# Optimization experiments

Measured on AMD Instinct MI355X. Metric: run time of the kernel, lower is better.

Reference implementation:

```python
import jax, jax.numpy as jnp
import numpy as np

B, S, D = 32, 512, 1024
H, HD = 16, 64          # num_heads, head_dim
K = 64                  # downsampling_k
NEG = -9e15             # -9000000000000000.0 in source


def setup_inputs() -> dict:
    key0 = jax.random.key(0)
    ks = jax.random.split(key0, 8)
    glorot = lambda k, shape, fan: jax.random.uniform(k, shape, jnp.float32,
                                                      -np.sqrt(6.0 / fan), np.sqrt(6.0 / fan))
    fan = D + H * HD  # glorot_uniform over (hidden, heads*head_dim)
    return {
        "query": jax.random.normal(ks[0], (B, S, D), jnp.float32),
        "key": jax.random.normal(ks[1], (B, S, D), jnp.float32),
        "value": jax.random.normal(ks[2], (B, S, D), jnp.float32),
        "query_kernel": glorot(ks[3], (D, H, HD), fan),
        "key_kernel": glorot(ks[4], (D, H, HD), fan),
        "value_kernel": glorot(ks[5], (D, H, HD), fan),
        "key_downsample_mat": (1.0 / K) * jax.random.normal(ks[6], (K, S), jnp.float32),
        "value_downsample_mat": (1.0 / K) * jax.random.normal(ks[7], (K, S), jnp.float32),
    }


def reference(query, key, value, query_kernel, key_kernel, value_kernel,
              key_downsample_mat, value_downsample_mat):
    # Linformer-style downsampling of K/V along the sequence axis: [B,S,D] -> [B,K,D]
    key_ds = jnp.einsum('ks,bsd->bkd', key_downsample_mat, key)
    val_ds = jnp.einsum('ks,bsd->bkd', value_downsample_mat, value)

    # Per-head projections
    q = jnp.einsum('bsd,dnh->bsnh', query, query_kernel)   # [B,S,H,HD]
    k = jnp.einsum('bkd,dnh->bknh', key_ds, key_kernel)    # [B,K,H,HD]
    v = jnp.einsum('bkd,dnh->bknh', val_ds, value_kernel)  # [B,K,H,HD]

    # Masked softmax attention over the downsampled key set
    scores = jnp.einsum('bqnh,bknh->bnqk', q, k)           # [B,H,S,K]
    # Source builds tril over [S, K_down] then slices first K cols (no-op here)
    mask = jnp.tril(jnp.ones((S, K), dtype=bool))          # [S,K], broadcasts over B,H
    scores = jnp.where(mask, scores, NEG)
    attn = jax.nn.softmax(scores, axis=-1)                 # dropout deterministic (train=False)

    a_v = jnp.einsum('bnqk,bknh->bqnh', attn, v)           # [B,S,H,HD]
    return a_v.reshape(B, S, H * HD)
```

## Files before the change

kernel.cpp:

```cpp
#include <hip/hip_runtime.h>
#include <stdint.h>

#define B_   32
#define S_   512
#define D_   1024
#define H_   16
#define HD_  64
#define KD_  64
#define NH_  1024

typedef __attribute__((ext_vector_type(8))) short short8;
typedef __attribute__((ext_vector_type(4))) float floatx4;

#define GAS __attribute__((address_space(1)))
#define LAS __attribute__((address_space(3)))

__device__ __forceinline__ ushort f2bf(float f) {
  uint32_t u = __float_as_uint(f);
  u = u + 0x7FFFu + ((u >> 16) & 1u);
  return (ushort)(u >> 16);
}

__device__ __forceinline__ float bf2f(ushort h) {
  return __uint_as_float(((uint32_t)h) << 16);
}

__device__ __forceinline__ void gload_lds16(const void* g, void* l) {
  __builtin_amdgcn_global_load_lds((const GAS uint32_t*)g, (LAS uint32_t*)l, 16, 0, 0);
}

#define BARRIER() asm volatile("s_barrier" ::: "memory")
#define WAITLGKM() asm volatile("s_waitcnt lgkmcnt(0)" ::: "memory")

__global__ __launch_bounds__(256) void cvt_split(const float* __restrict__ kdm,
                                                 const float* __restrict__ vdm,
                                                 ushort* __restrict__ hi,
                                                 ushort* __restrict__ lo) {
  int i = blockIdx.x * 256 + threadIdx.x;
  const float* src = (i < 8192) ? kdm : vdm;
  int j = i & 8191;
  float4 v = ((const float4*)src)[j];
  ushort4 h, l;
  h.x = f2bf(v.x); l.x = f2bf(v.x - bf2f(h.x));
  h.y = f2bf(v.y); l.y = f2bf(v.y - bf2f(h.y));
  h.z = f2bf(v.z); l.z = f2bf(v.z - bf2f(h.z));
  h.w = f2bf(v.w); l.w = f2bf(v.w - bf2f(h.w));
  ((ushort4*)hi)[i] = h;
  ((ushort4*)lo)[i] = l;
}

__global__ __launch_bounds__(256, 6) void pre_kv(
    const float* __restrict__ key, const float* __restrict__ value,
    const float* __restrict__ kkm, const float* __restrict__ vkm,
    const ushort* __restrict__ dsm_hi, const ushort* __restrict__ dsm_lo,
    ushort* __restrict__ kkT, ushort* __restrict__ vkT,
    ushort* __restrict__ outk, ushort* __restrict__ outv) {
  __shared__ __align__(16) char smem[26624];
  const int blk = blockIdx.x;
  const int tid = threadIdx.x;

  if (blk < 512) {
    const int bz = (blk & 7) + ((blk >> 6) << 3);
    const int t  = (blk >> 3) & 7;
    const int z = bz >> 5, b = bz & 31;
    const int c0 = t * 128;
    const float* in = z ? value : key;
    ushort* out     = z ? outv : outk;
    const ushort* Ah = dsm_hi + (size_t)z * (KD_ * S_);
    const ushort* Al = dsm_lo + (size_t)z * (KD_ * S_);

    ushort* lAh = (ushort*)smem;
    ushort* lAl = (ushort*)(smem + 4096);
    uint*   lBh = (uint*)(smem + 8192);
    uint*   lBl = (uint*)(smem + 17408);

    const int lane = tid & 63, w = tid >> 6;
    const int lr = lane & 15, lg = lane >> 4;
    const int wn = w * 32;
    const int lam = tid & 31;
    const int d0 = lam * 4;
    const int sp = tid >> 5;

    floatx4 acc[4][2];
#pragma unroll
    for (int m = 0; m < 4; ++m)
#pragma unroll
      for (int n = 0; n < 2; ++n) acc[m][n] = (floatx4){0.f, 0.f, 0.f, 0.f};

    for (int k0 = 0; k0 < S_; k0 += 32) {
      {
        size_t src = (size_t)(tid >> 2) * S_ + k0 + (size_t)(tid & 3) * 8;
        gload_lds16(Ah + src, lAh + w * 512);
        gload_lds16(Al + src, lAl + w * 512);
      }
      float4 ra[2], rb[2];
#pragma unroll
      for (int si = 0; si < 2; ++si) {
        int s = sp * 2 + si * 16;
        const float* p = in + ((size_t)(b * S_ + k0 + s)) * D_ + c0 + d0;
        ra[si] = *(const float4*)p;
        rb[si] = *(const float4*)(p + D_);
      }
      const int swz = lam & 12;
#pragma unroll
      for (int si = 0; si < 2; ++si) {
        int col = (sp + si * 8) ^ swz;
        const float* pa = (const float*)&ra[si];
        const float* pb = (const float*)&rb[si];
#pragma unroll
        for (int i = 0; i < 4; ++i) {
          ushort h0 = f2bf(pa[i]);
          ushort l0 = f2bf(pa[i] - bf2f(h0));
          ushort h1 = f2bf(pb[i]);
          ushort l1 = f2bf(pb[i] - bf2f(h1));
          lBh[(d0 + i) * 18 + col] = (uint)h0 | ((uint)h1 << 16);
          lBl[(d0 + i) * 18 + col] = (uint)l0 | ((uint)l1 << 16);
        }
      }
      __syncthreads();
      short8 bh[2], bl[2];
#pragma unroll
      for (int n = 0; n < 2; ++n) {
        int d = wn + n * 16 + lr;
        int off = d * 18 + ((lg * 4) ^ ((d >> 2) & 12));
        bh[n] = *(const short8*)&lBh[off];
        bl[n] = *(const short8*)&lBl[off];
      }
#pragma unroll
      for (int m = 0; m < 4; ++m) {
        int aoff = (m * 16 + lr) * 32 + lg * 8;
        short8 ah = *(const short8*)&lAh[aoff];
        short8 al = *(const short8*)&lAl[aoff];
#pragma unroll
        for (int n = 0; n < 2; ++n) {
          acc[m][n] = __builtin_amdgcn_mfma_f32_16x16x32_bf16(ah, bh[n], acc[m][n], 0, 0, 0);
          acc[m][n] = __builtin_amdgcn_mfma_f32_16x16x32_bf16(ah, bl[n], acc[m][n], 0, 0, 0);
          acc[m][n] = __builtin_amdgcn_mfma_f32_16x16x32_bf16(al, bh[n], acc[m][n], 0, 0, 0);
        }
      }
      __syncthreads();
    }
    size_t obase = (size_t)b * KD_ * D_;
#pragma unroll
    for (int m = 0; m < 4; ++m)
#pragma unroll
      for (int n = 0; n < 2; ++n)
#pragma unroll
        for (int r = 0; r < 4; ++r)
          out[obase + (size_t)(m * 16 + lg * 4 + r) * D_ + c0 + wn + n * 16 + lr] =
              f2bf(acc[m][n][r]);

  } else {
    const int blk2 = blk - 512;
    const int tz = blk2 >> 10;
    const int rem = blk2 & 1023;
    const int tyb = rem >> 5;
    const int txb = rem & 31;
    const float* in = tz == 0 ? kkm : vkm;
    ushort* outp    = tz == 0 ? kkT : vkT;
    float (*tile)[33] = (float(*)[33])smem;
    const int tx = tid & 31, ty = tid >> 5;
    int x = txb * 32 + tx;
    int y0 = tyb * 32;
#pragma unroll
    for (int j = 0; j < 4; ++j)
      tile[ty + j * 8][tx] = in[(size_t)(y0 + ty + j * 8) * 1024 + x];
    __syncthreads();
    int x2 = tyb * 32 + tx;
    int y2 = txb * 32;
#pragma unroll
    for (int j = 0; j < 4; ++j)
      outp[(size_t)(y2 + ty + j * 8) * 1024 + x2] = f2bf(tile[tx][ty + j * 8]);
  }
}

__global__ __launch_bounds__(256) void gemm_kv_q(
    const ushort* __restrict__ A,
    const ushort* __restrict__ Bt,
    const ushort* __restrict__ Bt2,
    ushort* __restrict__ C,
    ushort* __restrict__ vpT,
    const float* __restrict__ qk, ushort* __restrict__ qkT,
    const float* __restrict__ query, ushort* __restrict__ q_bf) {
  __shared__ __align__(16) char smem[16384];
  const int blk = blockIdx.x;
  const int tid = threadIdx.x;

  if (blk < 256) {
    ushort* lA = (ushort*)smem;
    ushort* lB = (ushort*)(smem + 8192);
    int xcd = blk & 7, slot = blk >> 3;
    int mt = xcd * 4 + (slot >> 3);
    int nt = slot & 7;
    int m0 = mt * 128, n0 = nt * 128;
    const ushort* Bsel = (mt >= 16) ? Bt2 : Bt;

    int lane = tid & 63, w = tid >> 6;
    int lr = lane & 15, lg = lane >> 4;
    int wm = (w >> 1) * 64, wn = (w & 1) * 64;
    floatx4 acc[4][4];
#pragma unroll
    for (int m = 0; m < 4; ++m)
#pragma unroll
      for (int n = 0; n < 4; ++n) acc[m][n] = (floatx4){0.f, 0.f, 0.f, 0.f};

    for (int k0 = 0; k0 < 1024; k0 += 32) {
#pragma unroll
      for (int i = 0; i < 2; ++i) {
        int c = i * 256 + w * 64 + lane;
        gload_lds16(A + ((size_t)(m0 + (c >> 2)) * 1024 + k0 + (c & 3) * 8),
                    &lA[(i * 256 + w * 64) * 8]);
        gload_lds16(Bsel + ((size_t)(n0 + (c >> 2)) * 1024 + k0 + (c & 3) * 8),
                    &lB[(i * 256 + w * 64) * 8]);
      }
      __syncthreads();
      short8 af[4], bfr[4];
#pragma unroll
      for (int m = 0; m < 4; ++m)
        af[m] = *(const short8*)&lA[(wm + m * 16 + lr) * 32 + lg * 8];
#pragma unroll
      for (int n = 0; n < 4; ++n)
        bfr[n] = *(const short8*)&lB[(wn + n * 16 + lr) * 32 + lg * 8];
#pragma unroll
      for (int m = 0; m < 4; ++m)
#pragma unroll
        for (int n = 0; n < 4; ++n)
          acc[m][n] = __builtin_amdgcn_mfma_f32_16x16x32_bf16(af[m], bfr[n], acc[m][n], 0, 0, 0);
      __syncthreads();
    }
    if (mt < 16) {
#pragma unroll
      for (int m = 0; m < 4; ++m)
#pragma unroll
        for (int n = 0; n < 4; ++n)
#pragma unroll
          for (int r = 0; r < 4; ++r)
            C[(size_t)(m0 + wm + m * 16 + lg * 4 + r) * 1024 + n0 + wn + n * 16 + lr] =
                f2bf(acc[m][n][r]);
    } else {
#pragma unroll
      for (int m = 0; m < 4; ++m)
#pragma unroll
        for (int n = 0; n < 4; ++n) {
          int rowV = m0 - 2048 + wm + m * 16 + lg * 4;
          int b = rowV >> 6, k = rowV & 63;
          int hd = n0 + wn + n * 16 + lr;
          ushort4 o;
          o.x = f2bf(acc[m][n][0]); o.y = f2bf(acc[m][n][1]);
          o.z = f2bf(acc[m][n][2]); o.w = f2bf(acc[m][n][3]);
          *(ushort4*)&vpT[(size_t)b * 65536 + (size_t)hd * 64 + k] = o;
        }
    }

  } else if (blk < 256 + 1024) {
    const int blk2 = blk - 256;
    const int tyb = blk2 >> 5;
    const int txb = blk2 & 31;
    float (*tile)[33] = (float(*)[33])smem;
    const int tx = tid & 31, ty = tid >> 5;
    int x = txb * 32 + tx;
    int y0 = tyb * 32;
#pragma unroll
    for (int j = 0; j < 4; ++j)
      tile[ty + j * 8][tx] = qk[(size_t)(y0 + ty + j * 8) * 1024 + x];
    __syncthreads();
    int x2 = tyb * 32 + tx;
    int y2 = txb * 32;
#pragma unroll
    for (int j = 0; j < 4; ++j)
      qkT[(size_t)(y2 + ty + j * 8) * 1024 + x2] = f2bf(tile[tx][ty + j * 8]);

  } else {
    const size_t base = (size_t)(blk - 1280) * 2048 + tid;
#pragma unroll
    for (int j = 0; j < 8; ++j) {
      size_t i = base + (size_t)j * 256;
      float4 v = ((const float4*)query)[i];
      ushort4 o;
      o.x = f2bf(v.x); o.y = f2bf(v.y); o.z = f2bf(v.z); o.w = f2bf(v.w);
      ((ushort4*)q_bf)[i] = o;
    }
  }
}

__global__ __launch_bounds__(512, 2) void gemm256_attn(
    const ushort* __restrict__ A, const ushort* __restrict__ Bt,
    const ushort* __restrict__ kp, const ushort* __restrict__ vpT,
    float* __restrict__ out) {
  extern __shared__ ushort lds[];
  ushort* ldsA = lds;
  ushort* ldsB = lds + 2 * 256 * 64;
  const int tid = threadIdx.x;
  const int w = tid >> 6, lane = tid & 63;
  const int lr = lane & 15, lg = lane >> 4;
  const int wm = w >> 2, wn = w & 3;
  const int bid = blockIdx.x;
  const int mt = (bid & 7) * 8 + ((bid >> 3) >> 2);
  const int nt = (bid >> 3) & 3;
  const int m0 = mt * 256, n0 = nt * 256;
  const int NT = 16;

  const int srow = tid >> 3;
  const int sslot = tid & 7;

  auto stageA = [&](int sl, int ch, int k0) {
    int rloc = ch * 64 + srow;
    int gs = sslot ^ (rloc & 7);
    gload_lds16(A + (size_t)(m0 + rloc) * 1024 + k0 + gs * 8,
                ldsA + sl * (256 * 64) + ch * (64 * 64) + w * 512);
  };
  auto stageB = [&](int sl, int ch, int k0) {
    int rloc = ch * 64 + srow;
    int gs = sslot ^ (rloc & 7);
    gload_lds16(Bt + (size_t)(n0 + rloc) * 1024 + k0 + gs * 8,
                ldsB + sl * (256 * 64) + ch * (64 * 64) + w * 512);
  };

  short8 af[4][2], bf[2][2];
  auto loadA = [&](int sl, int mh) {
#pragma unroll
    for (int i = 0; i < 4; ++i) {
      int row = wm * 128 + (mh * 4 + i) * 16 + lr;
#pragma unroll
      for (int kk = 0; kk < 2; ++kk) {
        int col = (((kk * 4 + lg) ^ (row & 7)) * 8);
        af[i][kk] = *(const short8*)&ldsA[sl * (256 * 64) + row * 64 + col];
      }
    }
  };
  auto loadB = [&](int sl, int nh) {
#pragma unroll
    for (int j = 0; j < 2; ++j) {
      int row = wn * 64 + (nh * 2 + j) * 16 + lr;
#pragma unroll
      for (int kk = 0; kk < 2; ++kk) {
        int col = (((kk * 4 + lg) ^ (row & 7)) * 8);
        bf[j][kk] = *(const short8*)&ldsB[sl * (256 * 64) + row * 64 + col];
      }
    }
  };

  floatx4 acc[8][4];
#pragma unroll
  for (int i = 0; i < 8; ++i)
#pragma unroll
    for (int j = 0; j < 4; ++j) acc[i][j] = (floatx4){0.f, 0.f, 0.f, 0.f};

  auto mma16 = [&](int mh, int nh) {
    __builtin_amdgcn_s_setprio(1);
#pragma unroll
    for (int i = 0; i < 4; ++i)
#pragma unroll
      for (int j = 0; j < 2; ++j)
#pragma unroll
        for (int kk = 0; kk < 2; ++kk)
          acc[mh * 4 + i][nh * 2 + j] = __builtin_amdgcn_mfma_f32_16x16x32_bf16(
              af[i][kk], bf[j][kk], acc[mh * 4 + i][nh * 2 + j], 0, 0, 0);
    __builtin_amdgcn_s_setprio(0);
  };

#pragma unroll
  for (int ch = 0; ch < 4; ++ch) { stageA(0, ch, 0); stageB(0, ch, 0); }

#pragma unroll 2
  for (int t = 0; t < NT; ++t) {
    const int s = t & 1, ns = s ^ 1;
    const int kn = (t + 1) << 6;
    const bool more = (t + 1 < NT);
    if (more) { stageA(ns, 0, kn); stageA(ns, 1, kn); }
    if (more) { asm volatile("s_waitcnt vmcnt(2)" ::: "memory"); }
    else      { asm volatile("s_waitcnt vmcnt(0)" ::: "memory"); }
    BARRIER();
    loadA(s, 0); loadB(s, 0);
    WAITLGKM();
    mma16(0, 0);
    BARRIER();
    loadB(s, 1);
    if (more) { stageB(ns, 0, kn); stageB(ns, 1, kn); }
    BARRIER();
    WAITLGKM();
    mma16(0, 1);
    BARRIER();
    loadA(s, 1);
    if (more) { stageA(ns, 2, kn); stageA(ns, 3, kn); }
    BARRIER();
    WAITLGKM();
    mma16(1, 1);
    BARRIER();
    loadB(s, 0);
    if (more) { stageB(ns, 2, kn); stageB(ns, 3, kn); }
    BARRIER();
    WAITLGKM();
    mma16(1, 0);
    BARRIER();
  }

  ushort* QP = lds + w * 4608;
  const int b = mt >> 1;
  const int hq = nt * 4 + wn;

#pragma unroll
  for (int half = 0; half < 2; ++half) {
    const int srow0 = (mt & 1) * 256 + wm * 128 + half * 64;
#pragma unroll
    for (int mi = 0; mi < 4; ++mi)
#pragma unroll
      for (int nj = 0; nj < 4; ++nj)
#pragma unroll
        for (int r = 0; r < 4; ++r)
          QP[(mi * 16 + lg * 4 + r) * 72 + nj * 16 + lr] =
              f2bf(acc[half * 4 + mi][nj][r]);
    WAITLGKM();
    __builtin_amdgcn_sched_barrier(0);
    floatx4 qacc[4][4];
#pragma unroll
    for (int m = 0; m < 4; ++m)
#pragma unroll
      for (int n = 0; n < 4; ++n) qacc[m][n] = (floatx4){0.f, 0.f, 0.f, 0.f};
#pragma unroll
    for (int kk = 0; kk < 2; ++kk) {
      short8 qa[4], kb[4];
#pragma unroll
      for (int m = 0; m < 4; ++m)
        qa[m] = *(const short8*)&QP[(m * 16 + lr) * 72 + kk * 32 + lg * 8];
#pragma unroll
      for (int n = 0; n < 4; ++n)
        kb[n] = *(const short8*)(kp + ((size_t)b * KD_ + n * 16 + lr) * 1024 +
                                 hq * HD_ + kk * 32 + lg * 8);
#pragma unroll
      for (int m = 0; m < 4; ++m)
#pragma unroll
        for (int n = 0; n < 4; ++n)
          qacc[m][n] = __builtin_amdgcn_mfma_f32_16x16x32_bf16(qa[m], kb[n], qacc[m][n], 0, 0, 0);
    }
#pragma unroll
    for (int m = 0; m < 4; ++m) {
#pragma unroll
      for (int r = 0; r < 4; ++r) {
        int srow2 = srow0 + m * 16 + lg * 4 + r;
        float vals[4];
        float mx = -1e30f;
#pragma unroll
        for (int n = 0; n < 4; ++n) {
          int col = n * 16 + lr;
          float val = qacc[m][n][r];
          val = (col <= srow2) ? val : -1e30f;
          vals[n] = val;
          mx = fmaxf(mx, val);
        }
        mx = fmaxf(mx, __shfl_xor(mx, 1));
        mx = fmaxf(mx, __shfl_xor(mx, 2));
        mx = fmaxf(mx, __shfl_xor(mx, 4));
        mx = fmaxf(mx, __shfl_xor(mx, 8));
        float sum = 0.f;
#pragma unroll
        for (int n = 0; n < 4; ++n) {
          float e = __expf(vals[n] - mx);
          vals[n] = e;
          sum += e;
        }
        sum += __shfl_xor(sum, 1);
        sum += __shfl_xor(sum, 2);
        sum += __shfl_xor(sum, 4);
        sum += __shfl_xor(sum, 8);
        float inv = 1.0f / sum;
#pragma unroll
        for (int n = 0; n < 4; ++n)
          QP[(m * 16 + lg * 4 + r) * 72 + n * 16 + lr] = f2bf(vals[n] * inv);
      }
    }
    WAITLGKM();
    __builtin_amdgcn_sched_barrier(0);
    floatx4 oacc[4][4];
#pragma unroll
    for (int m = 0; m < 4; ++m)
#pragma unroll
      for (int n = 0; n < 4; ++n) oacc[m][n] = (floatx4){0.f, 0.f, 0.f, 0.f};
#pragma unroll
    for (int kk = 0; kk < 2; ++kk) {
      short8 pa[4], vb[4];
#pragma unroll
      for (int m = 0; m < 4; ++m)
        pa[m] = *(const short8*)&QP[(m * 16 + lr) * 72 + kk * 32 + lg * 8];
#pragma unroll
      for (int n = 0; n < 4; ++n)
        vb[n] = *(const short8*)(vpT + (size_t)b * 65536 +
                                 (size_t)(hq * HD_ + n * 16 + lr) * 64 +
                                 kk * 32 + lg * 8);
#pragma unroll
      for (int m = 0; m < 4; ++m)
#pragma unroll
        for (int n = 0; n < 4; ++n)
          oacc[m][n] = __builtin_amdgcn_mfma_f32_16x16x32_bf16(pa[m], vb[n], oacc[m][n], 0, 0, 0);
    }
#pragma unroll
    for (int m = 0; m < 4; ++m)
#pragma unroll
      for (int n = 0; n < 4; ++n)
#pragma unroll
        for (int r = 0; r < 4; ++r)
          out[((size_t)b * S_ + srow0 + m * 16 + lg * 4 + r) * 1024 +
              hq * HD_ + n * 16 + lr] = oacc[m][n][r];
  }
}

extern "C" void kernel_launch(void* const* d_in, const int* in_sizes, int n_in,
                              void* d_out, int out_size, void* d_ws, size_t ws_size,
                              hipStream_t stream) {
  const float* query = (const float*)d_in[0];
  const float* key   = (const float*)d_in[1];
  const float* value = (const float*)d_in[2];
  const float* qk    = (const float*)d_in[3];
  const float* kk    = (const float*)d_in[4];
  const float* vk    = (const float*)d_in[5];
  const float* kdm   = (const float*)d_in[6];
  const float* vdm   = (const float*)d_in[7];
  float* out = (float*)d_out;

  char* ws = (char*)d_ws;
  if (ws_size < (90ull << 20)) return;
  ushort* q_bf   = (ushort*)(ws);
  ushort* qkT    = (ushort*)(ws + (33ull << 20));
  ushort* kkT    = (ushort*)(ws + (35ull << 20));
  ushort* vkT    = (ushort*)(ws + (37ull << 20));
  ushort* kds    = (ushort*)(ws + (39ull << 20));
  ushort* vds    = (ushort*)(ws + (43ull << 20));
  ushort* k_proj = (ushort*)(ws + (79ull << 20));
  ushort* v_projT= (ushort*)(ws + (83ull << 20));
  ushort* dsm_hi = (ushort*)(ws + (87ull << 20));
  ushort* dsm_lo = (ushort*)(ws + (87ull << 20) + (128ull << 10));

  hipFuncSetAttribute((const void*)gemm256_attn,
                      hipFuncAttributeMaxDynamicSharedMemorySize, 131072);

  cvt_split<<<64, 256, 0, stream>>>(kdm, vdm, dsm_hi, dsm_lo);
  pre_kv<<<512 + 2048, 256, 0, stream>>>(
      key, value, kk, vk, dsm_hi, dsm_lo, kkT, vkT, kds, vds);
  gemm_kv_q<<<256 + 1024 + 2048, 256, 0, stream>>>(
      kds, kkT, vkT, k_proj, v_projT, qk, qkT, query, q_bf);
  gemm256_attn<<<256, 512, 131072, stream>>>(q_bf, qkT, k_proj, v_projT, out);
}
```

Baseline: 128.2 us.

## Halve pre_kv downsample tile width and prefetch next key/value slab into registers

The downsampling GEMM in pre_kv now gives each block 64 output columns instead of 128, so twice as many blocks run with a smaller LDS footprint and fewer accumulators per thread. The fp32 key/value loads for the next k-step are issued before the current step's MFMAs, with explicit vmcnt waits and raw barriers, so global latency overlaps with compute. The aim is more parallelism and occupancy and hidden load latency. In exchange the dsm hi/lo tiles are reloaded twice as often, and the hand-written waitcnt logic carries correctness risk.

```diff
diff --git a/kernel.cpp b/kernel.cpp
--- a/kernel.cpp
+++ b/kernel.cpp
@@ -55,15 +55,15 @@
     const ushort* __restrict__ dsm_hi, const ushort* __restrict__ dsm_lo,
     ushort* __restrict__ kkT, ushort* __restrict__ vkT,
     ushort* __restrict__ outk, ushort* __restrict__ outv) {
-  __shared__ __align__(16) char smem[26624];
+  __shared__ __align__(16) char smem[17408];
   const int blk = blockIdx.x;
   const int tid = threadIdx.x;
 
-  if (blk < 512) {
-    const int bz = (blk & 7) + ((blk >> 6) << 3);
-    const int t  = (blk >> 3) & 7;
+  if (blk < 1024) {
+    const int bz = (blk & 7) + ((blk >> 7) << 3);
+    const int t  = (blk >> 3) & 15;
     const int z = bz >> 5, b = bz & 31;
-    const int c0 = t * 128;
+    const int c0 = t * 64;
     const float* in = z ? value : key;
     ushort* out     = z ? outv : outk;
     const ushort* Ah = dsm_hi + (size_t)z * (KD_ * S_);
@@ -72,20 +72,23 @@
     ushort* lAh = (ushort*)smem;
     ushort* lAl = (ushort*)(smem + 4096);
     uint*   lBh = (uint*)(smem + 8192);
-    uint*   lBl = (uint*)(smem + 17408);
+    uint*   lBl = (uint*)(smem + 12800);
 
     const int lane = tid & 63, w = tid >> 6;
     const int lr = lane & 15, lg = lane >> 4;
-    const int wn = w * 32;
-    const int lam = tid & 31;
+    const int wn = w * 16;
+    const int lam = tid & 15;
     const int d0 = lam * 4;
-    const int sp = tid >> 5;
-
-    floatx4 acc[4][2];
-#pragma unroll
-    for (int m = 0; m < 4; ++m)
-#pragma unroll
-      for (int n = 0; n < 2; ++n) acc[m][n] = (floatx4){0.f, 0.f, 0.f, 0.f};
+    const int sp = tid >> 4;
+    const int swz = lam & 12;
+
+    floatx4 acc[4];
+#pragma unroll
+    for (int m = 0; m < 4; ++m) acc[m] = (floatx4){0.f, 0.f, 0.f, 0.f};
+
+    const float* pbase = in + (size_t)b * S_ * D_ + c0 + d0;
+    float4 ra = *(const float4*)(pbase + (size_t)(sp * 2) * D_);
+    float4 rb = *(const float4*)(pbase + (size_t)(sp * 2 + 1) * D_);
 
     for (int k0 = 0; k0 < S_; k0 += 32) {
       {
@@ -93,20 +96,10 @@
         gload_lds16(Ah + src, lAh + w * 512);
         gload_lds16(Al + src, lAl + w * 512);
       }
-      float4 ra[2], rb[2];
-#pragma unroll
-      for (int si = 0; si < 2; ++si) {
-        int s = sp * 2 + si * 16;
-        const float* p = in + ((size_t)(b * S_ + k0 + s)) * D_ + c0 + d0;
-        ra[si] = *(const float4*)p;
-        rb[si] = *(const float4*)(p + D_);
-      }
-      const int swz = lam & 12;
-#pragma unroll
-      for (int si = 0; si < 2; ++si) {
-        int col = (sp + si * 8) ^ swz;
-        const float* pa = (const float*)&ra[si];
-        const float* pb = (const float*)&rb[si];
+      {
+        int col = sp ^ swz;
+        const float* pa = (const float*)&ra;
+        const float* pb = (const float*)&rb;
 #pragma unroll
         for (int i = 0; i < 4; ++i) {
           ushort h0 = f2bf(pa[i]);
@@ -117,41 +110,44 @@
           lBl[(d0 + i) * 18 + col] = (uint)l0 | ((uint)l1 << 16);
         }
       }
-      __syncthreads();
-      short8 bh[2], bl[2];
-#pragma unroll
-      for (int n = 0; n < 2; ++n) {
-        int d = wn + n * 16 + lr;
+      if (k0 + 32 < S_) {
+        const float* pn = pbase + (size_t)(k0 + 32) * D_;
+        ra = *(const float4*)(pn + (size_t)(sp * 2) * D_);
+        rb = *(const float4*)(pn + (size_t)(sp * 2 + 1) * D_);
+        asm volatile("s_waitcnt vmcnt(2)" ::: "memory");
+      } else {
+        asm volatile("s_waitcnt vmcnt(0)" ::: "memory");
+      }
+      WAITLGKM();
+      BARRIER();
+      short8 bh, bl;
+      {
+        int d = wn + lr;
         int off = d * 18 + ((lg * 4) ^ ((d >> 2) & 12));
-        bh[n] = *(const short8*)&lBh[off];
-        bl[n] = *(const short8*)&lBl[off];
+        bh = *(const short8*)&lBh[off];
+        bl = *(const short8*)&lBl[off];
       }
 #pragma unroll
       for (int m = 0; m < 4; ++m) {
         int aoff = (m * 16 + lr) * 32 + lg * 8;
         short8 ah = *(const short8*)&lAh[aoff];
         short8 al = *(const short8*)&lAl[aoff];
-#pragma unroll
-        for (int n = 0; n < 2; ++n) {
-          acc[m][n] = __builtin_amdgcn_mfma_f32_16x16x32_bf16(ah, bh[n], acc[m][n], 0, 0, 0);
-          acc[m][n] = __builtin_amdgcn_mfma_f32_16x16x32_bf16(ah, bl[n], acc[m][n], 0, 0, 0);
-          acc[m][n] = __builtin_amdgcn_mfma_f32_16x16x32_bf16(al, bh[n], acc[m][n], 0, 0, 0);
-        }
-      }
-      __syncthreads();
+        acc[m] = __builtin_amdgcn_mfma_f32_16x16x32_bf16(ah, bh, acc[m], 0, 0, 0);
+        acc[m] = __builtin_amdgcn_mfma_f32_16x16x32_bf16(ah, bl, acc[m], 0, 0, 0);
+        acc[m] = __builtin_amdgcn_mfma_f32_16x16x32_bf16(al, bh, acc[m], 0, 0, 0);
+      }
+      BARRIER();
     }
     size_t obase = (size_t)b * KD_ * D_;
 #pragma unroll
     for (int m = 0; m < 4; ++m)
 #pragma unroll
-      for (int n = 0; n < 2; ++n)
-#pragma unroll
-        for (int r = 0; r < 4; ++r)
-          out[obase + (size_t)(m * 16 + lg * 4 + r) * D_ + c0 + wn + n * 16 + lr] =
-              f2bf(acc[m][n][r]);
+      for (int r = 0; r < 4; ++r)
+        out[obase + (size_t)(m * 16 + lg * 4 + r) * D_ + c0 + wn + lr] =
+            f2bf(acc[m][r]);
 
   } else {
-    const int blk2 = blk - 512;
+    const int blk2 = blk - 1024;
     const int tz = blk2 >> 10;
     const int rem = blk2 & 1023;
     const int tyb = rem >> 5;
@@ -534,7 +530,7 @@
                       hipFuncAttributeMaxDynamicSharedMemorySize, 131072);
 
   cvt_split<<<64, 256, 0, stream>>>(kdm, vdm, dsm_hi, dsm_lo);
-  pre_kv<<<512 + 2048, 256, 0, stream>>>(
+  pre_kv<<<1024 + 2048, 256, 0, stream>>>(
       key, value, kk, vk, dsm_hi, dsm_lo, kkT, vkT, kds, vds);
   gemm_kv_q<<<256 + 1024 + 2048, 256, 0, stream>>>(
       kds, kkT, vkT, k_proj, v_projT, qk, qkT, query, q_bf);
```

Result: no change. 129.4 us (+0.9%).
